# Performance work log

Measured on AMD Instinct MI355X. Metric: run time of the kernel, lower is better.

## Reference

```python
import jax, jax.numpy as jnp
import numpy as np

NUM_HEADS = 16
TOP_K = 2

def setup_inputs() -> dict:
    key = jax.random.key(0)
    ks = jax.random.split(key, 5)
    B, D, E = 8192, 2048, 8
    x = jax.random.normal(ks[0], (B, D), dtype=jnp.float32)
    W_qkv = jax.random.normal(ks[1], (E, D, 3 * D), dtype=jnp.float32) * 0.02  # (in,out) per expert
    W_gate = jax.random.normal(ks[2], (D, E), dtype=jnp.float32) * 0.02
    b_gate = jnp.zeros((E,), dtype=jnp.float32)
    W_proj = jax.random.normal(ks[3], (D, D), dtype=jnp.float32) * 0.02
    b_proj = jnp.zeros((D,), dtype=jnp.float32)
    return {"x": x, "W_qkv": W_qkv, "W_gate": W_gate, "b_gate": b_gate,
            "W_proj": W_proj, "b_proj": b_proj}


def reference(x, W_qkv, W_gate, b_gate, W_proj, b_proj):
    B, D = x.shape
    E = W_qkv.shape[0]
    H = NUM_HEADS
    hd = D // H
    scale = float(hd) ** -0.5

    # gating + top-k (sparse gate weights, zeros for non-selected experts)
    gate_scores = jax.nn.softmax(x @ W_gate + b_gate, axis=-1)        # (B, E)
    topk_vals, topk_idx = jax.lax.top_k(gate_scores, TOP_K)           # (B, K)
    gw = jnp.zeros_like(gate_scores).at[jnp.arange(B)[:, None], topk_idx].add(topk_vals)

    # gate-weighted combine of expert QKV projections (linear => combine after GEMM)
    qkv = jnp.zeros((B, 3 * D), dtype=x.dtype)
    for e in range(E):  # fixed small expert count; each iter is one big GEMM
        qkv = qkv + gw[:, e:e + 1] * (x @ W_qkv[e])
    qkv = qkv.reshape(B, 3, H, hd)

    # NOTE: the torch source writes `q = k = v = torch.zeros(...)` then uses
    # in-place `+=`, so q, k, v ALIAS one tensor: all equal gate*(q_i+k_i+v_i).
    # We replicate that exact math faithfully.
    s = qkv.sum(axis=1)                                               # (B, H, hd)

    attn = jax.nn.softmax(jnp.einsum('bhd,bgd->bhg', s, s) * scale, axis=-1)  # (B, H, H)
    out = jnp.einsum('bhg,bgd->bhd', attn, s)                         # (B, H, hd)
    out = out.transpose(0, 2, 1).reshape(B, D)                        # matches .transpose(1,2).reshape
    return out @ W_proj + b_proj
```

## Files before the change

kernel.cpp:

```cpp
#include <hip/hip_runtime.h>

#define B_ROWS 8192
#define DDIM 2048
#define NEXP 8
#define NASSIGN (B_ROWS * 2)
#define MAX_TILES 80

typedef unsigned short u16;
typedef short bf16x8 __attribute__((ext_vector_type(8)));
typedef float f32x4 __attribute__((ext_vector_type(4)));

#define M_CNT 0
#define M_FILL 8
#define M_SEG 16
#define M_CTRA 24
#define M_CTRB 32
#define M_NT 40
#define M_TE 48
#define M_TB 128
#define M_TR 208

__device__ __forceinline__ u16 f2b(float f) {
  union { float f; unsigned u; } c; c.f = f;
  return (u16)((c.u + 0x7fffu + ((c.u >> 16) & 1u)) >> 16);
}
__device__ __forceinline__ float b2f(u16 h) {
  union { unsigned u; float f; } c; c.u = ((unsigned)h) << 16;
  return c.f;
}
__device__ __forceinline__ void async16(u16* lds, const u16* g) {
  __builtin_amdgcn_global_load_lds(
      (const __attribute__((address_space(1))) unsigned int*)g,
      (__attribute__((address_space(3))) unsigned int*)lds, 16, 0, 0);
}

__global__ void init_meta_kernel(int* meta) {
  int t = threadIdx.x;
  if (t < 48) meta[t] = 0;
}

template <int NSUM>
__global__ __launch_bounds__(256) void prep_transpose(
    const float* __restrict__ Win, u16* __restrict__ Wout, int ldin) {
  __shared__ u16 tl[64][72];
  int bx = blockIdx.x;
  int nt = bx & 31, kt = (bx >> 5) & 31, e = bx >> 10;
  int t = threadIdx.x;
  const size_t in_base = (size_t)e * DDIM * (size_t)ldin;
  int k0 = kt * 64, n0 = nt * 64;
#pragma unroll
  for (int i = 0; i < 4; ++i) {
    int idx = i * 256 + t;
    int kl = idx >> 4, f4 = idx & 15;
    const float* p = Win + in_base + (size_t)(k0 + kl) * ldin + n0 + f4 * 4;
    float4 v = *(const float4*)p;
    if (NSUM == 3) {
      float4 v1 = *(const float4*)(p + 2048);
      float4 v2 = *(const float4*)(p + 4096);
      v.x += v1.x + v2.x; v.y += v1.y + v2.y;
      v.z += v1.z + v2.z; v.w += v1.w + v2.w;
    }
    tl[f4 * 4 + 0][kl] = f2b(v.x);
    tl[f4 * 4 + 1][kl] = f2b(v.y);
    tl[f4 * 4 + 2][kl] = f2b(v.z);
    tl[f4 * 4 + 3][kl] = f2b(v.w);
  }
  __syncthreads();
  u16* out = Wout + (size_t)e * DDIM * DDIM;
#pragma unroll
  for (int i = 0; i < 2; ++i) {
    int idx = i * 256 + t;
    int nl = idx >> 3, kc = idx & 7;
    const u16* r = &tl[nl][kc * 8];
    uint4 pk;
    pk.x = (unsigned)r[0] | ((unsigned)r[1] << 16);
    pk.y = (unsigned)r[2] | ((unsigned)r[3] << 16);
    pk.z = (unsigned)r[4] | ((unsigned)r[5] << 16);
    pk.w = (unsigned)r[6] | ((unsigned)r[7] << 16);
    *(uint4*)(out + (size_t)(n0 + nl) * DDIM + k0 + kc * 8) = pk;
  }
}

__global__ __launch_bounds__(256) void gate_kernel(
    const float* __restrict__ x, const float* __restrict__ Wg,
    const float* __restrict__ bg, u16* __restrict__ xb,
    int* __restrict__ e01, float* __restrict__ w01, int* __restrict__ meta) {
  int b = blockIdx.x, t = threadIdx.x;
  const float* xr = x + (size_t)b * DDIM;
  float4 v0 = ((const float4*)xr)[2 * t];
  float4 v1 = ((const float4*)xr)[2 * t + 1];
  float xv[8] = {v0.x, v0.y, v0.z, v0.w, v1.x, v1.y, v1.z, v1.w};
  uint4 pk;
  pk.x = (unsigned)f2b(xv[0]) | ((unsigned)f2b(xv[1]) << 16);
  pk.y = (unsigned)f2b(xv[2]) | ((unsigned)f2b(xv[3]) << 16);
  pk.z = (unsigned)f2b(xv[4]) | ((unsigned)f2b(xv[5]) << 16);
  pk.w = (unsigned)f2b(xv[6]) | ((unsigned)f2b(xv[7]) << 16);
  *(uint4*)(xb + (size_t)b * DDIM + t * 8) = pk;

  double acc[8] = {0, 0, 0, 0, 0, 0, 0, 0};
#pragma unroll
  for (int j = 0; j < 8; ++j) {
    const float4* wr = (const float4*)(Wg + (size_t)(t * 8 + j) * 8);
    float4 wa = wr[0], wb = wr[1];
    double xd = (double)xv[j];
    acc[0] += xd * wa.x; acc[1] += xd * wa.y;
    acc[2] += xd * wa.z; acc[3] += xd * wa.w;
    acc[4] += xd * wb.x; acc[5] += xd * wb.y;
    acc[6] += xd * wb.z; acc[7] += xd * wb.w;
  }
#pragma unroll
  for (int e = 0; e < 8; ++e)
    for (int m2 = 32; m2; m2 >>= 1) acc[e] += __shfl_xor(acc[e], m2);
  __shared__ double red[4][8];
  if ((t & 63) == 0)
    for (int e = 0; e < 8; ++e) red[t >> 6][e] = acc[e];
  __syncthreads();
  if (t == 0) {
    double l[8];
    for (int e = 0; e < 8; ++e)
      l[e] = red[0][e] + red[1][e] + red[2][e] + red[3][e] + (double)bg[e];
    double mx = l[0];
    for (int e = 1; e < 8; ++e) mx = l[e] > mx ? l[e] : mx;
    double p[8], s = 0;
    for (int e = 0; e < 8; ++e) { p[e] = exp(l[e] - mx); s += p[e]; }
    int i1 = 0;
    for (int e = 1; e < 8; ++e) if (p[e] > p[i1]) i1 = e;
    int i2 = (i1 == 0) ? 1 : 0;
    for (int e = 0; e < 8; ++e)
      if (e != i1 && p[e] > p[i2]) i2 = e;
    e01[2 * b] = i1; e01[2 * b + 1] = i2;
    w01[2 * b] = (float)(p[i1] / s);
    w01[2 * b + 1] = (float)(p[i2] / s);
    atomicAdd(&meta[M_CNT + i1], 1);
    atomicAdd(&meta[M_CNT + i2], 1);
  }
}

__global__ __launch_bounds__(128) void scan_kernel(int* meta) {
  __shared__ int scnt[8];
  int t = threadIdx.x;
  if (t < 8) scnt[t] = meta[M_CNT + t];
  __syncthreads();
  int seg[9], pre[9];
  seg[0] = 0; pre[0] = 0;
#pragma unroll
  for (int e = 0; e < 8; ++e) {
    seg[e + 1] = seg[e] + scnt[e];
    pre[e + 1] = pre[e] + ((scnt[e] + 255) >> 8);
  }
  if (t < 8) meta[M_SEG + t] = seg[t];
  if (t == 0) meta[M_NT] = pre[8];
  if (t < MAX_TILES) {
    if (t < pre[8]) {
      int e = 0;
      while (e < 7 && t >= pre[e + 1]) ++e;
      int i = t - pre[e];
      meta[M_TE + t] = e;
      meta[M_TB + t] = seg[e] + i * 256;
      meta[M_TR + t] = scnt[e] - i * 256;
    } else {
      meta[M_TE + t] = 0; meta[M_TB + t] = 0; meta[M_TR + t] = 0;
    }
  }
}

__global__ __launch_bounds__(256) void build_kernel(
    const int* __restrict__ e01, const float* __restrict__ w01,
    int* __restrict__ meta, int* __restrict__ rows, float* __restrict__ wt,
    int* __restrict__ rowpos) {
  int b = blockIdx.x * 256 + threadIdx.x;
  if (b >= B_ROWS) return;
#pragma unroll
  for (int s = 0; s < 2; ++s) {
    int e = e01[2 * b + s];
    float w = w01[2 * b + s];
    int p = meta[M_SEG + e] + atomicAdd(&meta[M_FILL + e], 1);
    rows[p] = b;
    wt[p] = w;
    rowpos[2 * b + s] = p;
  }
}

#define BAR() __builtin_amdgcn_s_barrier()
#define VMCNT8() asm volatile("s_waitcnt vmcnt(8)" ::: "memory")
#define VMCNT0() asm volatile("s_waitcnt vmcnt(0)" ::: "memory")
#define LGKM_DRAIN() asm volatile("s_waitcnt lgkmcnt(0)" ::: "memory")

#define STAGE_A(L, T, BB) async16(&lds[BB][0][(L)*4096 + t * 8], srcA[L] + (size_t)(T)*64)
#define STAGE_B(L, T, BB) async16(&lds[BB][1][(L)*4096 + t * 8], srcB[L] + (size_t)(T)*64)

#define READ_A(QM)                                                   \
  do {                                                               \
    _Pragma("unroll") for (int i_ = 0; i_ < 4; ++i_) {               \
      int rb_ = baseA + ((QM)*64 + i_ * 16) * 128;                   \
      af[i_][0] = *(const bf16x8*)(pA + rb_ + ck0);                  \
      af[i_][1] = *(const bf16x8*)(pA + rb_ + ck1);                  \
    }                                                                \
  } while (0)
#define READ_B(H)                                                    \
  do {                                                               \
    _Pragma("unroll") for (int j_ = 0; j_ < 2; ++j_) {               \
      int rb_ = baseB + (((H)*2 + j_) * 16) * 128;                   \
      bfr[(H)*2 + j_][0] = *(const bf16x8*)(pB + rb_ + ck0);         \
      bfr[(H)*2 + j_][1] = *(const bf16x8*)(pB + rb_ + ck1);         \
    }                                                                \
  } while (0)
#define MFMA16(QM, QN)                                                         \
  do {                                                                         \
    _Pragma("unroll") for (int i_ = 0; i_ < 4; ++i_) {                         \
      _Pragma("unroll") for (int j_ = 0; j_ < 2; ++j_) {                       \
        acc[(QM)*4 + i_][(QN)*2 + j_] = __builtin_amdgcn_mfma_f32_16x16x32_bf16( \
            af[i_][0], bfr[(QN)*2 + j_][0], acc[(QM)*4 + i_][(QN)*2 + j_], 0, 0, 0); \
        acc[(QM)*4 + i_][(QN)*2 + j_] = __builtin_amdgcn_mfma_f32_16x16x32_bf16( \
            af[i_][1], bfr[(QN)*2 + j_][1], acc[(QM)*4 + i_][(QN)*2 + j_], 0, 0, 0); \
      }                                                                        \
    }                                                                          \
  } while (0)

template <int MODE>
__global__ __launch_bounds__(512, 2) void gemm256_kernel(
    const u16* __restrict__ A, const u16* __restrict__ BT,
    int* __restrict__ meta, const int* __restrict__ rows,
    const float* __restrict__ wt, const float* __restrict__ bias,
    u16* __restrict__ Yc, float* __restrict__ Out) {
  __shared__ __align__(16) u16 lds[2][2][16384];
  __shared__ int s_w;

  const int t = threadIdx.x;
  const int lane = t & 63;
  const int wid = t >> 6;
  const int wr = wid >> 2, wc = wid & 3;
  const int l15 = lane & 15;
  const int kg = lane >> 4;
  const int sw = lane & 7;
  const int baseA = (wr * 128 + l15) * 128;
  const int baseB = (wc * 64 + l15) * 128;
  const int ck0 = ((0 * 4 + kg) ^ sw) << 4;
  const int ck1 = ((1 * 4 + kg) ^ sw) << 4;

  const int nt = (MODE == 0) ? meta[M_NT] : 32;
  const int ctrbase = (MODE == 0) ? M_CTRA : M_CTRB;

  int xcd;
  asm volatile("s_getreg_b32 %0, hwreg(20, 0, 4)" : "=s"(xcd));
  xcd &= 7;

  int q = 0;

  for (;;) {
    if (t == 0) {
      int pk = -1;
      while (q < 8) {
        int qq = (xcd + q) & 7;
        int tlo_ = (qq * nt) >> 3;
        int cnt_ = (((qq + 1) * nt) >> 3) - tlo_;
        int w = atomicAdd(&meta[ctrbase + qq], 1);
        if (w < cnt_ * 8) { pk = (qq << 16) | w; break; }
        ++q;
      }
      s_w = pk;
    }
    __syncthreads();
    const int pk = s_w;
    if (pk < 0) return;
    const int qq = pk >> 16, w = pk & 0xffff;
    const int tlo = (qq * nt) >> 3;
    const int cnt = (((qq + 1) * nt) >> 3) - tlo;
    const int fp = cnt >> 1;
    int mt, n0i;
    if (w < fp * 16) {
      mt = tlo + ((w >> 4) << 1) + (w & 1);
      n0i = (w >> 1) & 7;
    } else {
      mt = tlo + cnt - 1;
      n0i = w - fp * 16;
    }
    const int n0 = n0i << 8;

    int e = 0, base = 0, rem = 256, m0 = 0;
    if (MODE == 0) {
      rem = meta[M_TR + mt];
      if (rem > 256) rem = 256;
      e = meta[M_TE + mt];
      base = meta[M_TB + mt];
    } else {
      m0 = mt << 8;
    }

    const u16* srcA[4];
    const u16* srcB[4];
#pragma unroll
    for (int L = 0; L < 4; ++L) {
      int row = L * 64 + (t >> 3);
      int cl = (t & 7) ^ (row & 7);
      int grow;
      if (MODE == 0) {
        int rl = row < rem ? row : 0;
        grow = rows[base + rl];
      } else {
        grow = m0 + row;
      }
      srcA[L] = A + (size_t)grow * DDIM + cl * 8;
      srcB[L] = BT + ((size_t)e * DDIM + n0 + row) * DDIM + cl * 8;
    }

    f32x4 acc[8][4];
#pragma unroll
    for (int i = 0; i < 8; ++i)
#pragma unroll
      for (int j = 0; j < 4; ++j) {
        f32x4 z = {0.f, 0.f, 0.f, 0.f};
        acc[i][j] = z;
      }

    bf16x8 af[4][2];
    bf16x8 bfr[4][2];

    STAGE_B(0, 0, 0); STAGE_B(1, 0, 0); STAGE_B(2, 0, 0); STAGE_B(3, 0, 0);
    STAGE_A(0, 0, 0); STAGE_A(1, 0, 0); STAGE_A(2, 0, 0); STAGE_A(3, 0, 0);
    STAGE_B(0, 1, 1); STAGE_B(1, 1, 1); STAGE_B(2, 1, 1); STAGE_B(3, 1, 1);
    STAGE_A(0, 1, 1); STAGE_A(1, 1, 1); STAGE_A(2, 1, 1); STAGE_A(3, 1, 1);
    VMCNT8();
    BAR();

    const int NT = DDIM / 64;
    for (int T = 0; T < NT; ++T) {
      const int cb = T & 1;
      const char* pA = (const char*)&lds[cb][0][0];
      const char* pB = (const char*)&lds[cb][1][0];
      READ_A(0);
      READ_B(0);
      BAR();
      __builtin_amdgcn_s_setprio(1);
      MFMA16(0, 0);
      __builtin_amdgcn_s_setprio(0);
      BAR();
      READ_B(1);
      BAR();
      __builtin_amdgcn_s_setprio(1);
      MFMA16(0, 1);
      __builtin_amdgcn_s_setprio(0);
      LGKM_DRAIN();
      BAR();
      READ_A(1);
      if (T + 2 < NT) {
        STAGE_B(0, T + 2, cb); STAGE_B(1, T + 2, cb);
        STAGE_B(2, T + 2, cb); STAGE_B(3, T + 2, cb);
      }
      BAR();
      __builtin_amdgcn_s_setprio(1);
      MFMA16(1, 0);
      __builtin_amdgcn_s_setprio(0);
      LGKM_DRAIN();
      BAR();
      if (T + 2 < NT) {
        STAGE_A(0, T + 2, cb); STAGE_A(1, T + 2, cb);
        STAGE_A(2, T + 2, cb); STAGE_A(3, T + 2, cb);
        VMCNT8();
      } else {
        VMCNT0();
      }
      BAR();
      __builtin_amdgcn_s_setprio(1);
      MFMA16(1, 1);
      __builtin_amdgcn_s_setprio(0);
      BAR();
    }

    if (MODE == 1) {
      float bv[4];
#pragma unroll
      for (int fn = 0; fn < 4; ++fn) bv[fn] = bias[n0 + wc * 64 + fn * 16 + l15];
#pragma unroll
      for (int qm = 0; qm < 2; ++qm)
#pragma unroll
        for (int i = 0; i < 4; ++i)
#pragma unroll
          for (int r = 0; r < 4; ++r) {
            int rl = wr * 128 + qm * 64 + i * 16 + kg * 4 + r;
            float* orow = Out + (size_t)(m0 + rl) * DDIM + n0 + wc * 64 + l15;
#pragma unroll
            for (int fn = 0; fn < 4; ++fn)
              orow[fn * 16] = acc[qm * 4 + i][fn][r] + bv[fn];
          }
    } else {
#pragma unroll
      for (int qm = 0; qm < 2; ++qm)
#pragma unroll
        for (int i = 0; i < 4; ++i)
#pragma unroll
          for (int r = 0; r < 4; ++r) {
            int rl = wr * 128 + qm * 64 + i * 16 + kg * 4 + r;
            if (rl < rem) {
              int pos = base + rl;
              float w2 = wt[pos];
              u16* yrow = Yc + (size_t)pos * DDIM + n0 + wc * 64 + l15;
#pragma unroll
              for (int fn = 0; fn < 4; ++fn)
                yrow[fn * 16] = f2b(w2 * acc[qm * 4 + i][fn][r]);
            }
          }
    }
  }
}

__global__ __launch_bounds__(256) void combine_attn_kernel(
    const u16* __restrict__ Yc, const int* __restrict__ rowpos,
    u16* __restrict__ ab) {
  __shared__ __align__(16) float sm[16][132];
  __shared__ float at[16][17];
  __shared__ __align__(16) float osm[16][132];
  int b = blockIdx.x, t = threadIdx.x;
  int p0 = rowpos[2 * b], p1 = rowpos[2 * b + 1];
  uint4 ya = *(const uint4*)(Yc + (size_t)p0 * DDIM + t * 8);
  uint4 yb = *(const uint4*)(Yc + (size_t)p1 * DDIM + t * 8);
  const unsigned* au = (const unsigned*)&ya;
  const unsigned* bu = (const unsigned*)&yb;
  float v[8];
#pragma unroll
  for (int j = 0; j < 4; ++j) {
    v[2 * j] = b2f((u16)(au[j] & 0xffff)) + b2f((u16)(bu[j] & 0xffff));
    v[2 * j + 1] = b2f((u16)(au[j] >> 16)) + b2f((u16)(bu[j] >> 16));
  }
  {
    int row = t >> 4, col = (t & 15) * 8;
    float4 w0 = {v[0], v[1], v[2], v[3]};
    float4 w1 = {v[4], v[5], v[6], v[7]};
    *(float4*)&sm[row][col] = w0;
    *(float4*)&sm[row][col + 4] = w1;
  }
  __syncthreads();
  const int h = t >> 4, g = t & 15;
  {
    const float4* sh4 = (const float4*)&sm[h][0];
    const float4* sg4 = (const float4*)&sm[g][0];
    float4 a4 = {0.f, 0.f, 0.f, 0.f};
#pragma unroll
    for (int j = 0; j < 32; ++j) {
      float4 xa = sh4[j], xc = sg4[j];
      a4.x += xa.x * xc.x; a4.y += xa.y * xc.y;
      a4.z += xa.z * xc.z; a4.w += xa.w * xc.w;
    }
    float dot = (a4.x + a4.y) + (a4.z + a4.w);
    float lg = dot * 0.088388347648318447f;
    float mx = lg;
#pragma unroll
    for (int m2 = 8; m2; m2 >>= 1) mx = fmaxf(mx, __shfl_xor(mx, m2, 16));
    float ex = expf(lg - mx);
    float sum = ex;
#pragma unroll
    for (int m2 = 8; m2; m2 >>= 1) sum += __shfl_xor(sum, m2, 16);
    at[h][g] = ex / sum;
  }
  __syncthreads();
  {
    const int c = t & 15;
    float4 o0 = {0.f, 0.f, 0.f, 0.f};
    float4 o1 = {0.f, 0.f, 0.f, 0.f};
#pragma unroll
    for (int gg = 0; gg < 16; ++gg) {
      float w = at[h][gg];
      float4 s0 = *(const float4*)&sm[gg][c * 4];
      float4 s1 = *(const float4*)&sm[gg][64 + c * 4];
      o0.x += w * s0.x; o0.y += w * s0.y; o0.z += w * s0.z; o0.w += w * s0.w;
      o1.x += w * s1.x; o1.y += w * s1.y; o1.z += w * s1.z; o1.w += w * s1.w;
    }
    *(float4*)&osm[h][c * 4] = o0;
    *(float4*)&osm[h][64 + c * 4] = o1;
  }
  __syncthreads();
  uint4 pk;
  unsigned w2[4];
#pragma unroll
  for (int j = 0; j < 4; ++j) {
    int f0 = t * 8 + 2 * j, f1 = t * 8 + 2 * j + 1;
    w2[j] = (unsigned)f2b(osm[f0 & 15][f0 >> 4]) |
            ((unsigned)f2b(osm[f1 & 15][f1 >> 4]) << 16);
  }
  pk.x = w2[0]; pk.y = w2[1]; pk.z = w2[2]; pk.w = w2[3];
  *(uint4*)(ab + (size_t)b * DDIM + t * 8) = pk;
}

extern "C" void kernel_launch(void* const* d_in, const int* in_sizes, int n_in,
                              void* d_out, int out_size, void* d_ws, size_t ws_size,
                              hipStream_t stream) {
  const float* x = (const float*)d_in[0];
  const float* Wqkv = (const float*)d_in[1];
  const float* Wg = (const float*)d_in[2];
  const float* bg = (const float*)d_in[3];
  const float* Wp = (const float*)d_in[4];
  const float* bp = (const float*)d_in[5];
  float* out = (float*)d_out;

  char* ws = (char*)d_ws;
  size_t off = 0;
  auto alloc = [&](size_t bytes) {
    void* p = ws + off;
    off += (bytes + 255) & ~(size_t)255;
    return p;
  };
  u16* xb = (u16*)alloc((size_t)B_ROWS * DDIM * 2);
  u16* WsumT = (u16*)alloc((size_t)NEXP * DDIM * DDIM * 2);
  u16* WprojT = (u16*)alloc((size_t)DDIM * DDIM * 2);
  u16* Yc = (u16*)alloc((size_t)NASSIGN * DDIM * 2);
  u16* ab = (u16*)alloc((size_t)B_ROWS * DDIM * 2);
  int* e01 = (int*)alloc((size_t)NASSIGN * 4);
  float* w01 = (float*)alloc((size_t)NASSIGN * 4);
  int* rows = (int*)alloc((size_t)NASSIGN * 4);
  float* wt = (float*)alloc((size_t)NASSIGN * 4);
  int* rowpos = (int*)alloc((size_t)NASSIGN * 4);
  int* meta = (int*)alloc(4096);

  init_meta_kernel<<<dim3(1), dim3(64), 0, stream>>>(meta);
  prep_transpose<3><<<dim3(NEXP * 32 * 32), dim3(256), 0, stream>>>(Wqkv, WsumT, 3 * DDIM);
  prep_transpose<1><<<dim3(32 * 32), dim3(256), 0, stream>>>(Wp, WprojT, DDIM);
  gate_kernel<<<dim3(B_ROWS), dim3(256), 0, stream>>>(x, Wg, bg, xb, e01, w01, meta);
  scan_kernel<<<dim3(1), dim3(128), 0, stream>>>(meta);
  build_kernel<<<dim3(32), dim3(256), 0, stream>>>(e01, w01, meta, rows, wt, rowpos);
  gemm256_kernel<0><<<dim3(256), dim3(512), 0, stream>>>(
      xb, WsumT, meta, rows, wt, nullptr, Yc, nullptr);
  combine_attn_kernel<<<dim3(B_ROWS), dim3(256), 0, stream>>>(Yc, rowpos, ab);
  gemm256_kernel<1><<<dim3(256), dim3(512), 0, stream>>>(
      ab, WprojT, meta, rows, wt, bp, nullptr, out);
  (void)in_sizes; (void)n_in; (void)out_size; (void)ws_size;
}
```

Baseline: 715.6 us.

## Replace 256x256 pipelined GEMM with simpler 128x128 single-buffered tile kernel

Shrinks the GEMM tile from 256x256 (512 threads, double-buffered LDS with staged prefetch and priority tricks) to 128x128 (256 threads, single LDS buffer, load-sync-compute loop). The scan metadata and the persistent work-stealing tile indexing are rescaled to match, so there are more, smaller tiles and higher occupancy. The goal is better load balance and less padding waste on the ragged per-expert tiles. In exchange it loses the overlap of global loads with MFMA work and data reuse per tile.

```diff
diff --git a/kernel.cpp b/kernel.cpp
--- a/kernel.cpp
+++ b/kernel.cpp
@@ -4,7 +4,7 @@
 #define DDIM 2048
 #define NEXP 8
 #define NASSIGN (B_ROWS * 2)
-#define MAX_TILES 80
+#define MAX_TILES 136
 
 typedef unsigned short u16;
 typedef short bf16x8 __attribute__((ext_vector_type(8)));
@@ -17,8 +17,8 @@
 #define M_CTRB 32
 #define M_NT 40
 #define M_TE 48
-#define M_TB 128
-#define M_TR 208
+#define M_TB 184
+#define M_TR 320
 
 __device__ __forceinline__ u16 f2b(float f) {
   union { float f; unsigned u; } c; c.f = f;
@@ -136,7 +136,7 @@
   }
 }
 
-__global__ __launch_bounds__(128) void scan_kernel(int* meta) {
+__global__ __launch_bounds__(256) void scan_kernel(int* meta) {
   __shared__ int scnt[8];
   int t = threadIdx.x;
   if (t < 8) scnt[t] = meta[M_CNT + t];
@@ -146,7 +146,7 @@
 #pragma unroll
   for (int e = 0; e < 8; ++e) {
     seg[e + 1] = seg[e] + scnt[e];
-    pre[e + 1] = pre[e] + ((scnt[e] + 255) >> 8);
+    pre[e + 1] = pre[e] + ((scnt[e] + 127) >> 7);
   }
   if (t < 8) meta[M_SEG + t] = seg[t];
   if (t == 0) meta[M_NT] = pre[8];
@@ -156,8 +156,8 @@
       while (e < 7 && t >= pre[e + 1]) ++e;
       int i = t - pre[e];
       meta[M_TE + t] = e;
-      meta[M_TB + t] = seg[e] + i * 256;
-      meta[M_TR + t] = scnt[e] - i * 256;
+      meta[M_TB + t] = seg[e] + i * 128;
+      meta[M_TR + t] = scnt[e] - i * 128;
     } else {
       meta[M_TE + t] = 0; meta[M_TB + t] = 0; meta[M_TR + t] = 0;
     }
@@ -181,69 +181,39 @@
   }
 }
 
-#define BAR() __builtin_amdgcn_s_barrier()
-#define VMCNT8() asm volatile("s_waitcnt vmcnt(8)" ::: "memory")
-#define VMCNT0() asm volatile("s_waitcnt vmcnt(0)" ::: "memory")
-#define LGKM_DRAIN() asm volatile("s_waitcnt lgkmcnt(0)" ::: "memory")
-
-#define STAGE_A(L, T, BB) async16(&lds[BB][0][(L)*4096 + t * 8], srcA[L] + (size_t)(T)*64)
-#define STAGE_B(L, T, BB) async16(&lds[BB][1][(L)*4096 + t * 8], srcB[L] + (size_t)(T)*64)
-
-#define READ_A(QM)                                                   \
-  do {                                                               \
-    _Pragma("unroll") for (int i_ = 0; i_ < 4; ++i_) {               \
-      int rb_ = baseA + ((QM)*64 + i_ * 16) * 128;                   \
-      af[i_][0] = *(const bf16x8*)(pA + rb_ + ck0);                  \
-      af[i_][1] = *(const bf16x8*)(pA + rb_ + ck1);                  \
-    }                                                                \
-  } while (0)
-#define READ_B(H)                                                    \
-  do {                                                               \
-    _Pragma("unroll") for (int j_ = 0; j_ < 2; ++j_) {               \
-      int rb_ = baseB + (((H)*2 + j_) * 16) * 128;                   \
-      bfr[(H)*2 + j_][0] = *(const bf16x8*)(pB + rb_ + ck0);         \
-      bfr[(H)*2 + j_][1] = *(const bf16x8*)(pB + rb_ + ck1);         \
-    }                                                                \
-  } while (0)
-#define MFMA16(QM, QN)                                                         \
-  do {                                                                         \
-    _Pragma("unroll") for (int i_ = 0; i_ < 4; ++i_) {                         \
-      _Pragma("unroll") for (int j_ = 0; j_ < 2; ++j_) {                       \
-        acc[(QM)*4 + i_][(QN)*2 + j_] = __builtin_amdgcn_mfma_f32_16x16x32_bf16( \
-            af[i_][0], bfr[(QN)*2 + j_][0], acc[(QM)*4 + i_][(QN)*2 + j_], 0, 0, 0); \
-        acc[(QM)*4 + i_][(QN)*2 + j_] = __builtin_amdgcn_mfma_f32_16x16x32_bf16( \
-            af[i_][1], bfr[(QN)*2 + j_][1], acc[(QM)*4 + i_][(QN)*2 + j_], 0, 0, 0); \
-      }                                                                        \
-    }                                                                          \
-  } while (0)
-
 template <int MODE>
-__global__ __launch_bounds__(512, 2) void gemm256_kernel(
+__global__ __launch_bounds__(256, 4) void gemm128_kernel(
     const u16* __restrict__ A, const u16* __restrict__ BT,
     int* __restrict__ meta, const int* __restrict__ rows,
     const float* __restrict__ wt, const float* __restrict__ bias,
     u16* __restrict__ Yc, float* __restrict__ Out) {
-  __shared__ __align__(16) u16 lds[2][2][16384];
+  __shared__ __align__(16) u16 ldsA[128 * 64];
+  __shared__ __align__(16) u16 ldsB[128 * 64];
   __shared__ int s_w;
 
   const int t = threadIdx.x;
   const int lane = t & 63;
   const int wid = t >> 6;
-  const int wr = wid >> 2, wc = wid & 3;
+  const int wr = wid >> 1, wc = wid & 1;
   const int l15 = lane & 15;
   const int kg = lane >> 4;
   const int sw = lane & 7;
-  const int baseA = (wr * 128 + l15) * 128;
-  const int baseB = (wc * 64 + l15) * 128;
-  const int ck0 = ((0 * 4 + kg) ^ sw) << 4;
-  const int ck1 = ((1 * 4 + kg) ^ sw) << 4;
-
-  const int nt = (MODE == 0) ? meta[M_NT] : 32;
+
+  const int nt = (MODE == 0) ? meta[M_NT] : 64;
   const int ctrbase = (MODE == 0) ? M_CTRA : M_CTRB;
 
   int xcd;
   asm volatile("s_getreg_b32 %0, hwreg(20, 0, 4)" : "=s"(xcd));
   xcd &= 7;
+
+  int aoff[4], boff[4];
+#pragma unroll
+  for (int i = 0; i < 4; ++i) {
+    aoff[i] = (wr * 64 + i * 16 + l15) * 128;
+    boff[i] = (wc * 64 + i * 16 + l15) * 128;
+  }
+  const int ck0 = (kg ^ sw) << 4;
+  const int ck1 = ((4 + kg) ^ sw) << 4;
 
   int q = 0;
 
@@ -255,7 +225,7 @@
         int tlo_ = (qq * nt) >> 3;
         int cnt_ = (((qq + 1) * nt) >> 3) - tlo_;
         int w = atomicAdd(&meta[ctrbase + qq], 1);
-        if (w < cnt_ * 8) { pk = (qq << 16) | w; break; }
+        if (w < cnt_ * 16) { pk = (qq << 16) | w; break; }
         ++q;
       }
       s_w = pk;
@@ -268,30 +238,30 @@
     const int cnt = (((qq + 1) * nt) >> 3) - tlo;
     const int fp = cnt >> 1;
     int mt, n0i;
-    if (w < fp * 16) {
-      mt = tlo + ((w >> 4) << 1) + (w & 1);
-      n0i = (w >> 1) & 7;
+    if (w < fp * 32) {
+      mt = tlo + ((w >> 5) << 1) + (w & 1);
+      n0i = (w >> 1) & 15;
     } else {
       mt = tlo + cnt - 1;
-      n0i = w - fp * 16;
-    }
-    const int n0 = n0i << 8;
-
-    int e = 0, base = 0, rem = 256, m0 = 0;
+      n0i = w - fp * 32;
+    }
+    const int n0 = n0i << 7;
+
+    int e = 0, base = 0, rem = 128, m0 = 0;
     if (MODE == 0) {
       rem = meta[M_TR + mt];
-      if (rem > 256) rem = 256;
+      if (rem > 128) rem = 128;
       e = meta[M_TE + mt];
       base = meta[M_TB + mt];
     } else {
-      m0 = mt << 8;
+      m0 = mt << 7;
     }
 
     const u16* srcA[4];
     const u16* srcB[4];
 #pragma unroll
     for (int L = 0; L < 4; ++L) {
-      int row = L * 64 + (t >> 3);
+      int row = L * 32 + (t >> 3);
       int cl = (t & 7) ^ (row & 7);
       int grow;
       if (MODE == 0) {
@@ -304,67 +274,44 @@
       srcB[L] = BT + ((size_t)e * DDIM + n0 + row) * DDIM + cl * 8;
     }
 
-    f32x4 acc[8][4];
-#pragma unroll
-    for (int i = 0; i < 8; ++i)
+    f32x4 acc[4][4];
+#pragma unroll
+    for (int i = 0; i < 4; ++i)
 #pragma unroll
       for (int j = 0; j < 4; ++j) {
         f32x4 z = {0.f, 0.f, 0.f, 0.f};
         acc[i][j] = z;
       }
 
-    bf16x8 af[4][2];
-    bf16x8 bfr[4][2];
-
-    STAGE_B(0, 0, 0); STAGE_B(1, 0, 0); STAGE_B(2, 0, 0); STAGE_B(3, 0, 0);
-    STAGE_A(0, 0, 0); STAGE_A(1, 0, 0); STAGE_A(2, 0, 0); STAGE_A(3, 0, 0);
-    STAGE_B(0, 1, 1); STAGE_B(1, 1, 1); STAGE_B(2, 1, 1); STAGE_B(3, 1, 1);
-    STAGE_A(0, 1, 1); STAGE_A(1, 1, 1); STAGE_A(2, 1, 1); STAGE_A(3, 1, 1);
-    VMCNT8();
-    BAR();
-
-    const int NT = DDIM / 64;
-    for (int T = 0; T < NT; ++T) {
-      const int cb = T & 1;
-      const char* pA = (const char*)&lds[cb][0][0];
-      const char* pB = (const char*)&lds[cb][1][0];
-      READ_A(0);
-      READ_B(0);
-      BAR();
-      __builtin_amdgcn_s_setprio(1);
-      MFMA16(0, 0);
-      __builtin_amdgcn_s_setprio(0);
-      BAR();
-      READ_B(1);
-      BAR();
-      __builtin_amdgcn_s_setprio(1);
-      MFMA16(0, 1);
-      __builtin_amdgcn_s_setprio(0);
-      LGKM_DRAIN();
-      BAR();
-      READ_A(1);
-      if (T + 2 < NT) {
-        STAGE_B(0, T + 2, cb); STAGE_B(1, T + 2, cb);
-        STAGE_B(2, T + 2, cb); STAGE_B(3, T + 2, cb);
+    const char* pA = (const char*)ldsA;
+    const char* pB = (const char*)ldsB;
+
+    for (int kt = 0; kt < 32; ++kt) {
+#pragma unroll
+      for (int L = 0; L < 4; ++L)
+        async16(&ldsA[(L * 256 + t) * 8], srcA[L] + kt * 64);
+#pragma unroll
+      for (int L = 0; L < 4; ++L)
+        async16(&ldsB[(L * 256 + t) * 8], srcB[L] + kt * 64);
+      __syncthreads();
+      bf16x8 af[4][2], bfr[4][2];
+#pragma unroll
+      for (int i = 0; i < 4; ++i) {
+        af[i][0] = *(const bf16x8*)(pA + aoff[i] + ck0);
+        af[i][1] = *(const bf16x8*)(pA + aoff[i] + ck1);
+        bfr[i][0] = *(const bf16x8*)(pB + boff[i] + ck0);
+        bfr[i][1] = *(const bf16x8*)(pB + boff[i] + ck1);
       }
-      BAR();
-      __builtin_amdgcn_s_setprio(1);
-      MFMA16(1, 0);
-      __builtin_amdgcn_s_setprio(0);
-      LGKM_DRAIN();
-      BAR();
-      if (T + 2 < NT) {
-        STAGE_A(0, T + 2, cb); STAGE_A(1, T + 2, cb);
-        STAGE_A(2, T + 2, cb); STAGE_A(3, T + 2, cb);
-        VMCNT8();
-      } else {
-        VMCNT0();
-      }
-      BAR();
-      __builtin_amdgcn_s_setprio(1);
-      MFMA16(1, 1);
-      __builtin_amdgcn_s_setprio(0);
-      BAR();
+#pragma unroll
+      for (int i = 0; i < 4; ++i)
+#pragma unroll
+        for (int j = 0; j < 4; ++j) {
+          acc[i][j] = __builtin_amdgcn_mfma_f32_16x16x32_bf16(
+              af[i][0], bfr[j][0], acc[i][j], 0, 0, 0);
+          acc[i][j] = __builtin_amdgcn_mfma_f32_16x16x32_bf16(
+              af[i][1], bfr[j][1], acc[i][j], 0, 0, 0);
+        }
+      __syncthreads();
     }
 
     if (MODE == 1) {
@@ -372,34 +319,30 @@
 #pragma unroll
       for (int fn = 0; fn < 4; ++fn) bv[fn] = bias[n0 + wc * 64 + fn * 16 + l15];
 #pragma unroll
-      for (int qm = 0; qm < 2; ++qm)
-#pragma unroll
-        for (int i = 0; i < 4; ++i)
-#pragma unroll
-          for (int r = 0; r < 4; ++r) {
-            int rl = wr * 128 + qm * 64 + i * 16 + kg * 4 + r;
-            float* orow = Out + (size_t)(m0 + rl) * DDIM + n0 + wc * 64 + l15;
+      for (int i = 0; i < 4; ++i)
+#pragma unroll
+        for (int r = 0; r < 4; ++r) {
+          int rl = wr * 64 + i * 16 + kg * 4 + r;
+          float* orow = Out + (size_t)(m0 + rl) * DDIM + n0 + wc * 64 + l15;
+#pragma unroll
+          for (int fn = 0; fn < 4; ++fn)
+            orow[fn * 16] = acc[i][fn][r] + bv[fn];
+        }
+    } else {
+#pragma unroll
+      for (int i = 0; i < 4; ++i)
+#pragma unroll
+        for (int r = 0; r < 4; ++r) {
+          int rl = wr * 64 + i * 16 + kg * 4 + r;
+          if (rl < rem) {
+            int pos = base + rl;
+            float w2 = wt[pos];
+            u16* yrow = Yc + (size_t)pos * DDIM + n0 + wc * 64 + l15;
 #pragma unroll
             for (int fn = 0; fn < 4; ++fn)
-              orow[fn * 16] = acc[qm * 4 + i][fn][r] + bv[fn];
+              yrow[fn * 16] = f2b(w2 * acc[i][fn][r]);
           }
-    } else {
-#pragma unroll
-      for (int qm = 0; qm < 2; ++qm)
-#pragma unroll
-        for (int i = 0; i < 4; ++i)
-#pragma unroll
-          for (int r = 0; r < 4; ++r) {
-            int rl = wr * 128 + qm * 64 + i * 16 + kg * 4 + r;
-            if (rl < rem) {
-              int pos = base + rl;
-              float w2 = wt[pos];
-              u16* yrow = Yc + (size_t)pos * DDIM + n0 + wc * 64 + l15;
-#pragma unroll
-              for (int fn = 0; fn < 4; ++fn)
-                yrow[fn * 16] = f2b(w2 * acc[qm * 4 + i][fn][r]);
-            }
-          }
+        }
     }
   }
 }
@@ -515,12 +458,12 @@
   prep_transpose<3><<<dim3(NEXP * 32 * 32), dim3(256), 0, stream>>>(Wqkv, WsumT, 3 * DDIM);
   prep_transpose<1><<<dim3(32 * 32), dim3(256), 0, stream>>>(Wp, WprojT, DDIM);
   gate_kernel<<<dim3(B_ROWS), dim3(256), 0, stream>>>(x, Wg, bg, xb, e01, w01, meta);
-  scan_kernel<<<dim3(1), dim3(128), 0, stream>>>(meta);
+  scan_kernel<<<dim3(1), dim3(256), 0, stream>>>(meta);
   build_kernel<<<dim3(32), dim3(256), 0, stream>>>(e01, w01, meta, rows, wt, rowpos);
-  gemm256_kernel<0><<<dim3(256), dim3(512), 0, stream>>>(
+  gemm128_kernel<0><<<dim3(1024), dim3(256), 0, stream>>>(
       xb, WsumT, meta, rows, wt, nullptr, Yc, nullptr);
   combine_attn_kernel<<<dim3(B_ROWS), dim3(256), 0, stream>>>(Yc, rowpos, ab);
-  gemm256_kernel<1><<<dim3(256), dim3(512), 0, stream>>>(
+  gemm128_kernel<1><<<dim3(1024), dim3(256), 0, stream>>>(
       ab, WprojT, meta, rows, wt, bp, nullptr, out);
   (void)in_sizes; (void)n_in; (void)out_size; (void)ws_size;
 }
```

Measured after the change: 801.2 us. 12.0% more time.
